# Performance work log

Hardware: AMD Instinct MI355X
Metric: run time of the kernel (lower is better)

Reference implementation:

```python
import jax, jax.numpy as jnp
import numpy as np

DIM = 512
CROSS_DIM = 512
NUM_HEADS = 8
DIM_HEAD = 64
INNER = NUM_HEADS * DIM_HEAD  # 512
SCALE = DIM_HEAD ** -0.5


def setup_inputs() -> dict:
    key = jax.random.key(0)
    ks = jax.random.split(key, 7)
    B, S, C = 2, 4096, 4096
    x = jax.random.normal(ks[0], (B, S, DIM), dtype=jnp.float32)
    context = jax.random.normal(ks[1], (B, C, CROSS_DIM), dtype=jnp.float32)
    # nn.Linear weights stored as [out, in]; we apply x @ W.T
    w_q = jax.random.normal(ks[2], (INNER, DIM), dtype=jnp.float32) * (DIM ** -0.5)
    w_k = jax.random.normal(ks[3], (INNER, CROSS_DIM), dtype=jnp.float32) * (CROSS_DIM ** -0.5)
    w_v = jax.random.normal(ks[4], (INNER, CROSS_DIM), dtype=jnp.float32) * (CROSS_DIM ** -0.5)
    w_out = jax.random.normal(ks[5], (DIM, INNER), dtype=jnp.float32) * (INNER ** -0.5)
    b_out = jax.random.normal(ks[6], (DIM,), dtype=jnp.float32) * 0.02
    return {"x": x, "context": context, "w_q": w_q, "w_k": w_k,
            "w_v": w_v, "w_out": w_out, "b_out": b_out}


def reference(x, context, w_q, w_k, w_v, w_out, b_out):
    B, S, _ = x.shape
    _, C, _ = context.shape
    # projections -> [B, H, L, Dh]
    q = (x @ w_q.T).reshape(B, S, NUM_HEADS, DIM_HEAD).transpose(0, 2, 1, 3)
    k = (context @ w_k.T).reshape(B, C, NUM_HEADS, DIM_HEAD).transpose(0, 2, 1, 3)
    v = (context @ w_v.T).reshape(B, C, NUM_HEADS, DIM_HEAD).transpose(0, 2, 1, 3)
    # scores [B, H, S, C]
    scores = jnp.einsum('bhsd,bhcd->bhsc', q, k) * SCALE
    attn = jax.nn.softmax(scores, axis=-1)
    out = jnp.einsum('bhsc,bhcd->bhsd', attn, v)  # [B,H,S,Dh]
    out = out.transpose(0, 2, 1, 3).reshape(B, S, INNER)
    return out @ w_out.T + b_out
```

## Files before the change

### kernel.cpp

```cpp
#include <hip/hip_runtime.h>

typedef __bf16 bf16;
typedef __bf16 bf16x2 __attribute__((ext_vector_type(2)));
typedef __bf16 bf16x4 __attribute__((ext_vector_type(4)));
typedef __bf16 bf16x8 __attribute__((ext_vector_type(8)));
typedef float  f32x4  __attribute__((ext_vector_type(4)));
typedef float  f32x16 __attribute__((ext_vector_type(16)));
typedef unsigned int uint4v __attribute__((ext_vector_type(4)));

#define MFMA16(a,b,c) __builtin_amdgcn_mfma_f32_16x16x32_bf16(a,b,c,0,0,0)
#define MFMA32(a,b,c) __builtin_amdgcn_mfma_f32_32x32x16_bf16(a,b,c,0,0,0)

__device__ __forceinline__ bf16x8 ld8_f32_to_bf16(const float* __restrict__ p)
{
    f32x4 a = *(const f32x4*)p;
    f32x4 b = *(const f32x4*)(p + 4);
    bf16x8 o;
#pragma unroll
    for (int j = 0; j < 4; j++) { o[j] = (bf16)a[j]; o[4 + j] = (bf16)b[j]; }
    return o;
}

__global__ __launch_bounds__(256, 2) void mm_qkv(
    const float* __restrict__ x,  const float* __restrict__ ctx,
    const float* __restrict__ wq, const float* __restrict__ wk,
    const float* __restrict__ wv,
    bf16* __restrict__ Qb, bf16* __restrict__ Kb, bf16* __restrict__ Vtb)
{
    __shared__ bf16 Al[128 * 40];
    __shared__ bf16 Wl[128 * 40];

    const float* A; const float* W; bf16* out; int mode;
    if (blockIdx.z == 0)      { A = x;   W = wq; out = Qb;  mode = 0; }
    else if (blockIdx.z == 1) { A = ctx; W = wk; out = Kb;  mode = 0; }
    else                      { A = ctx; W = wv; out = Vtb; mode = 1; }

    const int tid  = threadIdx.x;
    const int lane = tid & 63;
    const int w    = tid >> 6;
    const int wr   = w >> 1, wc = w & 1;
    const int bx   = blockIdx.x, by = blockIdx.y;
    const int q    = lane >> 4, m0 = lane & 15;

    f32x4 acc[4][4];
#pragma unroll
    for (int i = 0; i < 4; i++)
#pragma unroll
        for (int j = 0; j < 4; j++)
#pragma unroll
            for (int r = 0; r < 4; r++) acc[i][j][r] = 0.f;

    const int r0 = tid >> 2;
    const int c0 = (tid & 3) * 8;
    const float* Ab = A + (size_t)(by * 128) * 512;
    const float* Wb = W + (size_t)(bx * 128) * 512;

    for (int k0 = 0; k0 < 512; k0 += 32) {
        *(bf16x8*)&Al[r0 * 40 + c0]        = ld8_f32_to_bf16(Ab + (size_t)r0 * 512 + k0 + c0);
        *(bf16x8*)&Al[(r0 + 64) * 40 + c0] = ld8_f32_to_bf16(Ab + (size_t)(r0 + 64) * 512 + k0 + c0);
        *(bf16x8*)&Wl[r0 * 40 + c0]        = ld8_f32_to_bf16(Wb + (size_t)r0 * 512 + k0 + c0);
        *(bf16x8*)&Wl[(r0 + 64) * 40 + c0] = ld8_f32_to_bf16(Wb + (size_t)(r0 + 64) * 512 + k0 + c0);
        __syncthreads();

        bf16x8 af[4], wf[4];
#pragma unroll
        for (int mt = 0; mt < 4; mt++)
            af[mt] = *(const bf16x8*)&Al[(wr * 64 + mt * 16 + m0) * 40 + q * 8];
#pragma unroll
        for (int nt = 0; nt < 4; nt++)
            wf[nt] = *(const bf16x8*)&Wl[(wc * 64 + nt * 16 + m0) * 40 + q * 8];
#pragma unroll
        for (int mt = 0; mt < 4; mt++)
#pragma unroll
            for (int nt = 0; nt < 4; nt++)
                acc[mt][nt] = MFMA16(af[mt], wf[nt], acc[mt][nt]);
        __syncthreads();
    }

#pragma unroll
    for (int nt = 0; nt < 4; nt++) {
        const int col = bx * 128 + wc * 64 + nt * 16 + m0;
#pragma unroll
        for (int mt = 0; mt < 4; mt++) {
#pragma unroll
            for (int r = 0; r < 4; r++) {
                const int row = by * 128 + wr * 64 + mt * 16 + q * 4 + r;
                const bf16 v16 = (bf16)acc[mt][nt][r];
                if (mode == 0) {
                    out[(size_t)row * 512 + col] = v16;
                } else {
                    const int bb = row >> 12, c = row & 4095;
                    const int hh = col >> 6,  d = col & 63;
                    out[(size_t)((bb * 8 + hh) * 64 + d) * 4096 + c] = v16;
                }
            }
        }
    }
}

__global__ __launch_bounds__(256, 2) void mm_oproj(
    const bf16* __restrict__ Ob, const float* __restrict__ wout,
    const float* __restrict__ bout, float* __restrict__ out)
{
    __shared__ bf16 Al[128 * 40];
    __shared__ bf16 Wl[128 * 40];

    const int tid  = threadIdx.x;
    const int lane = tid & 63;
    const int w    = tid >> 6;
    const int wr   = w >> 1, wc = w & 1;
    const int bx   = blockIdx.x, by = blockIdx.y;
    const int q    = lane >> 4, m0 = lane & 15;

    f32x4 acc[4][4];
#pragma unroll
    for (int i = 0; i < 4; i++)
#pragma unroll
        for (int j = 0; j < 4; j++)
#pragma unroll
            for (int r = 0; r < 4; r++) acc[i][j][r] = 0.f;

    const int r0 = tid >> 2;
    const int c0 = (tid & 3) * 8;
    const bf16*  Ab = Ob   + (size_t)(by * 128) * 512;
    const float* Wb = wout + (size_t)(bx * 128) * 512;

    for (int k0 = 0; k0 < 512; k0 += 32) {
        *(bf16x8*)&Al[r0 * 40 + c0]        = *(const bf16x8*)(Ab + (size_t)r0 * 512 + k0 + c0);
        *(bf16x8*)&Al[(r0 + 64) * 40 + c0] = *(const bf16x8*)(Ab + (size_t)(r0 + 64) * 512 + k0 + c0);
        *(bf16x8*)&Wl[r0 * 40 + c0]        = ld8_f32_to_bf16(Wb + (size_t)r0 * 512 + k0 + c0);
        *(bf16x8*)&Wl[(r0 + 64) * 40 + c0] = ld8_f32_to_bf16(Wb + (size_t)(r0 + 64) * 512 + k0 + c0);
        __syncthreads();

        bf16x8 af[4], wf[4];
#pragma unroll
        for (int mt = 0; mt < 4; mt++)
            af[mt] = *(const bf16x8*)&Al[(wr * 64 + mt * 16 + m0) * 40 + q * 8];
#pragma unroll
        for (int nt = 0; nt < 4; nt++)
            wf[nt] = *(const bf16x8*)&Wl[(wc * 64 + nt * 16 + m0) * 40 + q * 8];
#pragma unroll
        for (int mt = 0; mt < 4; mt++)
#pragma unroll
            for (int nt = 0; nt < 4; nt++)
                acc[mt][nt] = MFMA16(af[mt], wf[nt], acc[mt][nt]);
        __syncthreads();
    }

#pragma unroll
    for (int nt = 0; nt < 4; nt++) {
        const int col = bx * 128 + wc * 64 + nt * 16 + m0;
        const float bv = bout[col];
#pragma unroll
        for (int mt = 0; mt < 4; mt++) {
#pragma unroll
            for (int r = 0; r < 4; r++) {
                const int row = by * 128 + wr * 64 + mt * 16 + q * 4 + r;
                out[(size_t)row * 512 + col] = acc[mt][nt][r] + bv;
            }
        }
    }
}

__global__ __launch_bounds__(256, 2) void fa_attn(
    const bf16* __restrict__ Qb, const bf16* __restrict__ Kb,
    const bf16* __restrict__ Vtb, bf16* __restrict__ Ob)
{
    __shared__ bf16 Kl[2][64 * 72];
    __shared__ bf16 Vl[2][64 * 72];

    const int tid  = threadIdx.x;
    const int lane = tid & 63;
    const int w    = tid >> 6;
    const int n0   = lane & 31;
    const int hd   = lane >> 5;
    const int b    = blockIdx.z, h0 = blockIdx.y;
    const int qg   = blockIdx.x * 128 + w * 32;

    bf16x8 qf[4];
    const bf16* qp = Qb + (size_t)(b * 4096 + qg + n0) * 512 + h0 * 64 + hd * 8;
#pragma unroll
    for (int ks = 0; ks < 4; ks++) {
        bf16x8 t = *(const bf16x8*)(qp + ks * 16);
#pragma unroll
        for (int j = 0; j < 8; j++) t[j] = (bf16)((float)t[j] * 0.125f);
        qf[ks] = t;
    }

    f32x16 oc[2];
#pragma unroll
    for (int dt = 0; dt < 2; dt++)
#pragma unroll
        for (int r = 0; r < 16; r++) oc[dt][r] = 0.f;
    float mrun = -1e30f, lrun = 0.f;

    const int srow = tid >> 2;
    const int scol = (tid & 3) * 16;
    const bf16* Kg = Kb  + (size_t)(b * 4096) * 512 + h0 * 64;
    const bf16* Vg = Vtb + (size_t)(b * 8 + h0) * 64 * 4096;

#define STAGE(buf, cb_) do { \
    *(bf16x8*)&Kl[buf][srow * 72 + scol]     = *(const bf16x8*)(Kg + (size_t)((cb_) + srow) * 512 + scol); \
    *(bf16x8*)&Kl[buf][srow * 72 + scol + 8] = *(const bf16x8*)(Kg + (size_t)((cb_) + srow) * 512 + scol + 8); \
    *(bf16x8*)&Vl[buf][srow * 72 + scol]     = *(const bf16x8*)(Vg + (size_t)srow * 4096 + (cb_) + scol); \
    *(bf16x8*)&Vl[buf][srow * 72 + scol + 8] = *(const bf16x8*)(Vg + (size_t)srow * 4096 + (cb_) + scol + 8); \
} while (0)

    STAGE(0, 0);
    int cur = 0;

    for (int cb = 0; cb < 4096; cb += 64) {
        __syncthreads();
        if (cb + 64 < 4096) STAGE(cur ^ 1, cb + 64);

        const bf16* Kc = &Kl[cur][0];
        const bf16* Vc = &Vl[cur][0];

        f32x16 st[2];
#pragma unroll
        for (int ct = 0; ct < 2; ct++) {
#pragma unroll
            for (int r = 0; r < 16; r++) st[ct][r] = 0.f;
#pragma unroll
            for (int ks = 0; ks < 4; ks++) {
                bf16x8 kf = *(const bf16x8*)&Kc[(ct * 32 + n0) * 72 + ks * 16 + hd * 8];
                st[ct] = MFMA32(kf, qf[ks], st[ct]);
            }
        }

        float mx = st[0][0];
#pragma unroll
        for (int ct = 0; ct < 2; ct++)
#pragma unroll
            for (int r = 0; r < 16; r++) mx = fmaxf(mx, st[ct][r]);
        mx = fmaxf(mx, __shfl_xor(mx, 32));

        const float mnew = fmaxf(mrun, mx);
        const float al = __expf(mrun - mnew);
        mrun = mnew;

        unsigned int pd[2][4][2];
        float rs = 0.f;
#pragma unroll
        for (int ct = 0; ct < 2; ct++)
#pragma unroll
            for (int g = 0; g < 4; g++)
#pragma unroll
                for (int t = 0; t < 2; t++) {
                    const float e0 = __expf(st[ct][4 * g + 2 * t]     - mnew);
                    const float e1 = __expf(st[ct][4 * g + 2 * t + 1] - mnew);
                    rs += e0 + e1;
                    bf16x2 pr; pr[0] = (bf16)e0; pr[1] = (bf16)e1;
                    pd[ct][g][t] = __builtin_bit_cast(unsigned int, pr);
                }
        rs += __shfl_xor(rs, 32);
        lrun = lrun * al + rs;
#pragma unroll
        for (int dt = 0; dt < 2; dt++)
#pragma unroll
            for (int r = 0; r < 16; r++) oc[dt][r] *= al;

#pragma unroll
        for (int ks = 0; ks < 4; ks++) {
            const int ct = ks >> 1;
            const int g0 = 2 * (ks & 1), g1 = g0 + 1;
            const unsigned int own0  = hd ? pd[ct][g1][0] : pd[ct][g0][0];
            const unsigned int own1  = hd ? pd[ct][g1][1] : pd[ct][g0][1];
            const unsigned int send0 = hd ? pd[ct][g0][0] : pd[ct][g1][0];
            const unsigned int send1 = hd ? pd[ct][g0][1] : pd[ct][g1][1];
            const unsigned int r0 = (unsigned int)__shfl_xor((int)send0, 32);
            const unsigned int r1 = (unsigned int)__shfl_xor((int)send1, 32);
            uint4v u;
            u[0] = hd ? r0 : own0;
            u[1] = hd ? r1 : own1;
            u[2] = hd ? own0 : r0;
            u[3] = hd ? own1 : r1;
            const bf16x8 pf = __builtin_bit_cast(bf16x8, u);
#pragma unroll
            for (int dt = 0; dt < 2; dt++) {
                bf16x8 vf = *(const bf16x8*)&Vc[(dt * 32 + n0) * 72 + ks * 16 + hd * 8];
                oc[dt] = MFMA32(vf, pf, oc[dt]);
            }
        }
        cur ^= 1;
    }
#undef STAGE

    const float rli = 1.0f / lrun;
    bf16* ob = Ob + (size_t)(b * 4096 + qg + n0) * 512 + h0 * 64;
#pragma unroll
    for (int dt = 0; dt < 2; dt++)
#pragma unroll
        for (int rq = 0; rq < 4; rq++) {
            bf16x4 o4;
#pragma unroll
            for (int i = 0; i < 4; i++) o4[i] = (bf16)(oc[dt][4 * rq + i] * rli);
            *(bf16x4*)&ob[dt * 32 + rq * 8 + hd * 4] = o4;
        }
}

__global__ void ws_sig11(float* out) { if (threadIdx.x == 0) out[0] = 777.0f; }

extern "C" void kernel_launch(void* const* d_in, const int* in_sizes, int n_in,
                              void* d_out, int out_size, void* d_ws, size_t ws_size,
                              hipStream_t stream)
{
    const float* x    = (const float*)d_in[0];
    const float* ctx  = (const float*)d_in[1];
    const float* wq   = (const float*)d_in[2];
    const float* wk   = (const float*)d_in[3];
    const float* wv   = (const float*)d_in[4];
    const float* wout = (const float*)d_in[5];
    const float* bout = (const float*)d_in[6];
    float* out = (float*)d_out;

    char* ws = (char*)d_ws;
    const size_t MB = 1024 * 1024;
    const size_t SZ = (size_t)8192 * 512 * sizeof(bf16);
    if (ws_size < 32 * MB) {
        ws_sig11<<<dim3(1), dim3(64), 0, stream>>>(out);
        return;
    }

    bf16* Qb  = (bf16*)(ws);
    bf16* Kb  = (bf16*)(ws + SZ);
    bf16* Vtb = (bf16*)(ws + 2 * SZ);
    bf16* Ob  = (bf16*)(ws + 3 * SZ);

    mm_qkv  <<<dim3(4, 64, 3), dim3(256), 0, stream>>>(x, ctx, wq, wk, wv, Qb, Kb, Vtb);
    fa_attn <<<dim3(32, 8, 2), dim3(256), 0, stream>>>(Qb, Kb, Vtb, Ob);
    mm_oproj<<<dim3(4, 64, 1), dim3(256), 0, stream>>>(Ob, wout, bout, out);
}
```

Measured before the change: 244.9 us.

## Split attention over context halves, add lazy softmax rescale and XCD-aware block remap

Attention is split along the context dimension into two halves when the workspace is large enough, which doubles the grid (1024 blocks) to raise occupancy on the many-CU device. Partial fp32 outputs and their (max, sum) statistics go to workspace, and a new merge kernel combines them. The online softmax now rescales only when the running max grows by more than 8, which skips most exp and multiply work per tile. All kernels also remap block indices so neighbouring tiles land on the same XCD, improving L2 reuse. The cost is extra fp32 traffic for the partials, one more kernel launch, and a somewhat larger range for the unnormalised exponentials.

```diff
diff --git a/kernel.cpp b/kernel.cpp
--- a/kernel.cpp
+++ b/kernel.cpp
@@ -30,16 +30,21 @@
     __shared__ bf16 Al[128 * 40];
     __shared__ bf16 Wl[128 * 40];
 
+    const int L  = blockIdx.x + 4 * (blockIdx.y + 64 * blockIdx.z);
+    const int L2 = (L & 7) * 96 + (L >> 3);
+    const int bx = L2 & 3;
+    const int by = (L2 >> 2) & 63;
+    const int z  = L2 >> 8;
+
     const float* A; const float* W; bf16* out; int mode;
-    if (blockIdx.z == 0)      { A = x;   W = wq; out = Qb;  mode = 0; }
-    else if (blockIdx.z == 1) { A = ctx; W = wk; out = Kb;  mode = 0; }
-    else                      { A = ctx; W = wv; out = Vtb; mode = 1; }
+    if (z == 0)      { A = x;   W = wq; out = Qb;  mode = 0; }
+    else if (z == 1) { A = ctx; W = wk; out = Kb;  mode = 0; }
+    else             { A = ctx; W = wv; out = Vtb; mode = 1; }
 
     const int tid  = threadIdx.x;
     const int lane = tid & 63;
     const int w    = tid >> 6;
     const int wr   = w >> 1, wc = w & 1;
-    const int bx   = blockIdx.x, by = blockIdx.y;
     const int q    = lane >> 4, m0 = lane & 15;
 
     f32x4 acc[4][4];
@@ -105,11 +110,15 @@
     __shared__ bf16 Al[128 * 40];
     __shared__ bf16 Wl[128 * 40];
 
+    const int L  = blockIdx.x + 4 * blockIdx.y;
+    const int L2 = (L & 7) * 32 + (L >> 3);
+    const int bx = L2 & 3;
+    const int by = L2 >> 2;
+
     const int tid  = threadIdx.x;
     const int lane = tid & 63;
     const int w    = tid >> 6;
     const int wr   = w >> 1, wc = w & 1;
-    const int bx   = blockIdx.x, by = blockIdx.y;
     const int q    = lane >> 4, m0 = lane & 15;
 
     f32x4 acc[4][4];
@@ -164,7 +173,8 @@
 
 __global__ __launch_bounds__(256, 2) void fa_attn(
     const bf16* __restrict__ Qb, const bf16* __restrict__ Kb,
-    const bf16* __restrict__ Vtb, bf16* __restrict__ Ob)
+    const bf16* __restrict__ Vtb, bf16* __restrict__ Ob,
+    float* __restrict__ Opart, float2* __restrict__ ml, const int nsplit)
 {
     __shared__ bf16 Kl[2][64 * 72];
     __shared__ bf16 Vl[2][64 * 72];
@@ -174,8 +184,19 @@
     const int w    = tid >> 6;
     const int n0   = lane & 31;
     const int hd   = lane >> 5;
-    const int b    = blockIdx.z, h0 = blockIdx.y;
-    const int qg   = blockIdx.x * 128 + w * 32;
+
+    const int nper = 64 * nsplit;
+    const int L  = blockIdx.x + 32 * (blockIdx.y + 8 * blockIdx.z);
+    const int L2 = (L & 7) * nper + (L >> 3);
+    const int qx = L2 & 31;
+    const int yz = L2 >> 5;
+    const int h0 = yz & 7;
+    const int zz = yz >> 3;
+    const int b  = (nsplit == 2) ? (zz >> 1) : zz;
+    const int ch = (nsplit == 2) ? (zz & 1) : 0;
+    const int clen = (nsplit == 2) ? 2048 : 4096;
+    const int c0 = ch * clen;
+    const int qg = qx * 128 + w * 32;
 
     bf16x8 qf[4];
     const bf16* qp = Qb + (size_t)(b * 4096 + qg + n0) * 512 + h0 * 64 + hd * 8;
@@ -206,12 +227,12 @@
     *(bf16x8*)&Vl[buf][srow * 72 + scol + 8] = *(const bf16x8*)(Vg + (size_t)srow * 4096 + (cb_) + scol + 8); \
 } while (0)
 
-    STAGE(0, 0);
+    STAGE(0, c0);
     int cur = 0;
 
-    for (int cb = 0; cb < 4096; cb += 64) {
+    for (int cb = c0; cb < c0 + clen; cb += 64) {
         __syncthreads();
-        if (cb + 64 < 4096) STAGE(cur ^ 1, cb + 64);
+        if (cb + 64 < c0 + clen) STAGE(cur ^ 1, cb + 64);
 
         const bf16* Kc = &Kl[cur][0];
         const bf16* Vc = &Vl[cur][0];
@@ -235,9 +256,16 @@
             for (int r = 0; r < 16; r++) mx = fmaxf(mx, st[ct][r]);
         mx = fmaxf(mx, __shfl_xor(mx, 32));
 
-        const float mnew = fmaxf(mrun, mx);
-        const float al = __expf(mrun - mnew);
-        mrun = mnew;
+        if (__any(mx > mrun + 8.f)) {
+            const float mnew = fmaxf(mrun, mx);
+            const float al = __expf(mrun - mnew);
+            mrun = mnew;
+            lrun *= al;
+#pragma unroll
+            for (int dt = 0; dt < 2; dt++)
+#pragma unroll
+                for (int r = 0; r < 16; r++) oc[dt][r] *= al;
+        }
 
         unsigned int pd[2][4][2];
         float rs = 0.f;
@@ -247,18 +275,14 @@
             for (int g = 0; g < 4; g++)
 #pragma unroll
                 for (int t = 0; t < 2; t++) {
-                    const float e0 = __expf(st[ct][4 * g + 2 * t]     - mnew);
-                    const float e1 = __expf(st[ct][4 * g + 2 * t + 1] - mnew);
+                    const float e0 = __expf(st[ct][4 * g + 2 * t]     - mrun);
+                    const float e1 = __expf(st[ct][4 * g + 2 * t + 1] - mrun);
                     rs += e0 + e1;
                     bf16x2 pr; pr[0] = (bf16)e0; pr[1] = (bf16)e1;
                     pd[ct][g][t] = __builtin_bit_cast(unsigned int, pr);
                 }
         rs += __shfl_xor(rs, 32);
-        lrun = lrun * al + rs;
-#pragma unroll
-        for (int dt = 0; dt < 2; dt++)
-#pragma unroll
-            for (int r = 0; r < 16; r++) oc[dt][r] *= al;
+        lrun += rs;
 
 #pragma unroll
         for (int ks = 0; ks < 4; ks++) {
@@ -286,17 +310,55 @@
     }
 #undef STAGE
 
-    const float rli = 1.0f / lrun;
-    bf16* ob = Ob + (size_t)(b * 4096 + qg + n0) * 512 + h0 * 64;
-#pragma unroll
-    for (int dt = 0; dt < 2; dt++)
-#pragma unroll
-        for (int rq = 0; rq < 4; rq++) {
-            bf16x4 o4;
-#pragma unroll
-            for (int i = 0; i < 4; i++) o4[i] = (bf16)(oc[dt][4 * rq + i] * rli);
-            *(bf16x4*)&ob[dt * 32 + rq * 8 + hd * 4] = o4;
-        }
+    if (nsplit == 1) {
+        const float rli = 1.0f / lrun;
+        bf16* ob = Ob + (size_t)(b * 4096 + qg + n0) * 512 + h0 * 64;
+#pragma unroll
+        for (int dt = 0; dt < 2; dt++)
+#pragma unroll
+            for (int rq = 0; rq < 4; rq++) {
+                bf16x4 o4;
+#pragma unroll
+                for (int i = 0; i < 4; i++) o4[i] = (bf16)(oc[dt][4 * rq + i] * rli);
+                *(bf16x4*)&ob[dt * 32 + rq * 8 + hd * 4] = o4;
+            }
+    } else {
+        float* Op = Opart + ((size_t)(ch * 2 + b) * 4096 + qg + n0) * 512 + h0 * 64;
+#pragma unroll
+        for (int dt = 0; dt < 2; dt++)
+#pragma unroll
+            for (int rq = 0; rq < 4; rq++) {
+                f32x4 o4;
+#pragma unroll
+                for (int i = 0; i < 4; i++) o4[i] = oc[dt][4 * rq + i];
+                *(f32x4*)&Op[dt * 32 + rq * 8 + hd * 4] = o4;
+            }
+        if (hd == 0)
+            ml[((size_t)(ch * 2 + b) * 8 + h0) * 4096 + qg + n0] = make_float2(mrun, lrun);
+    }
+}
+
+__global__ __launch_bounds__(256) void fa_merge(
+    const float* __restrict__ Opart, const float2* __restrict__ ml,
+    bf16* __restrict__ Ob)
+{
+    const int e   = blockIdx.x * 256 + threadIdx.x;
+    const int row = e >> 7;
+    const int c4  = (e & 127) * 4;
+    const int b   = row >> 12, sr = row & 4095, h = c4 >> 6;
+
+    const float2 u = ml[((size_t)(0 + b) * 8 + h) * 4096 + sr];
+    const float2 v = ml[((size_t)(2 + b) * 8 + h) * 4096 + sr];
+    const float m  = fmaxf(u.x, v.x);
+    const float w1 = __expf(u.x - m), w2 = __expf(v.x - m);
+    const float rL = 1.0f / (u.y * w1 + v.y * w2);
+
+    const f32x4 o1 = *(const f32x4*)&Opart[((size_t)(0 + b) * 4096 + sr) * 512 + c4];
+    const f32x4 o2 = *(const f32x4*)&Opart[((size_t)(2 + b) * 4096 + sr) * 512 + c4];
+    bf16x4 o;
+#pragma unroll
+    for (int i = 0; i < 4; i++) o[i] = (bf16)((o1[i] * w1 + o2[i] * w2) * rL);
+    *(bf16x4*)&Ob[(size_t)row * 512 + c4] = o;
 }
 
 __global__ void ws_sig11(float* out) { if (threadIdx.x == 0) out[0] = 777.0f; }
@@ -327,7 +389,13 @@
     bf16* Vtb = (bf16*)(ws + 2 * SZ);
     bf16* Ob  = (bf16*)(ws + 3 * SZ);
 
+    const int nsplit = (ws_size >= 66 * MB) ? 2 : 1;
+    float*  Opart = (float*)(ws + 32 * MB);
+    float2* mlp   = (float2*)(ws + 64 * MB);
+
     mm_qkv  <<<dim3(4, 64, 3), dim3(256), 0, stream>>>(x, ctx, wq, wk, wv, Qb, Kb, Vtb);
-    fa_attn <<<dim3(32, 8, 2), dim3(256), 0, stream>>>(Qb, Kb, Vtb, Ob);
+    fa_attn <<<dim3(32, 8, 2 * nsplit), dim3(256), 0, stream>>>(Qb, Kb, Vtb, Ob, Opart, mlp, nsplit);
+    if (nsplit == 2)
+        fa_merge<<<dim3(4096), dim3(256), 0, stream>>>(Opart, mlp, Ob);
     mm_oproj<<<dim3(4, 64, 1), dim3(256), 0, stream>>>(Ob, wout, bout, out);
 }
```

After: 246.5 us. No clear change (+0.6%).
